# Kernel tuning notes

Measured on AMD Instinct MI355X. Metric: run time of the kernel, lower is better.

Reference implementation:

```python
import jax, jax.numpy as jnp
import numpy as np

B = 256
NUM_IN_CAPS = 1152   # 6*6*32
NUM_OUT_CAPS = 10
VEC_IN = 8
VEC_OUT = 16
ROUTING_ITERS = 3


def squash(x, axis):
    # squash(v) = |v|^2/(1+|v|^2) * v/|v|  (matches torch module, no eps)
    mag_squ = jnp.sum(x * x, axis=axis, keepdims=True)
    return mag_squ / (1.0 + mag_squ) * (x / jnp.sqrt(mag_squ))


def setup_inputs() -> dict:
    key = jax.random.key(0)
    k = jax.random.split(key, 6)
    x = jax.random.normal(k[0], (B, 1, 28, 28), dtype=jnp.float32)
    conv1_w = jax.random.normal(k[1], (256, 1, 9, 9), dtype=jnp.float32) * 0.1
    conv1_b = jnp.zeros((256,), dtype=jnp.float32)
    pc_w = jax.random.normal(k[2], (256, 256, 9, 9), dtype=jnp.float32) * 0.02  # out = 32 caps * 8 dims
    pc_b = jnp.zeros((256,), dtype=jnp.float32)
    # routing transform W: original shape [1,1152,160,8,1] -> [1152,10,16,8]
    W = jax.random.normal(k[3], (NUM_IN_CAPS, NUM_OUT_CAPS, VEC_OUT, VEC_IN), dtype=jnp.float32)
    dc_bias = jnp.zeros((NUM_OUT_CAPS, VEC_OUT), dtype=jnp.float32)
    return {"x": x, "conv1_w": conv1_w, "conv1_b": conv1_b,
            "pc_w": pc_w, "pc_b": pc_b, "W": W, "dc_bias": dc_bias}


def _conv(x, w, b, stride):
    y = jax.lax.conv_general_dilated(x, w, (stride, stride), 'VALID',
                                     dimension_numbers=('NCHW', 'OIHW', 'NCHW'))
    return y + b[None, :, None, None]


def reference(x, conv1_w, conv1_b, pc_w, pc_b, W, dc_bias):
    # conv1: [B,1,28,28] -> [B,256,20,20]  (no activation in original module)
    h = _conv(x, conv1_w, conv1_b, stride=1)
    # primaryCaps conv: -> [B,256,6,6] -> [B,1152,8]
    caps = _conv(h, pc_w, pc_b, stride=2)
    caps = caps.reshape(caps.shape[0], -1, VEC_IN)          # [B,1152,8]
    caps = squash(caps, axis=-1)
    # u_hat[b,i,j,d] = sum_k W[i,j,d,k] * caps[b,i,k]  (the original broadcast-mul-sum)
    u_hat = jnp.einsum('ijdk,bik->bijd', W, caps)           # [B,1152,10,16]
    b_ij = jnp.zeros(u_hat.shape[:3], dtype=u_hat.dtype)    # [B,1152,10]
    for r in range(ROUTING_ITERS):
        c_ij = jax.nn.softmax(b_ij, axis=2)                 # softmax over output caps
        s_j = jnp.einsum('bij,bijd->bjd', c_ij, u_hat) + dc_bias  # [B,10,16]
        v_j = squash(s_j, axis=-1)
        if r != ROUTING_ITERS - 1:
            b_ij = b_ij + jnp.einsum('bijd,bjd->bij', u_hat, v_j)
    return v_j  # [B,10,16]
```

## Files before the change

kernel.cpp:

```cpp
#include <hip/hip_runtime.h>
#include <hip/hip_bf16.h>


typedef __attribute__((ext_vector_type(8))) short short8;
typedef __attribute__((ext_vector_type(4))) float float4v;

__device__ inline float bfu(ushort v){ return __uint_as_float((unsigned)v << 16); }

__global__ __launch_bounds__(640) void conv1_kernel(const float* __restrict__ x,
    const float* __restrict__ w, const float* __restrict__ bias,
    __hip_bfloat16* __restrict__ ht){
  __shared__ float img[784];
  __shared__ float wsv[32 * 81];
  __shared__ ushort tile[400 * 33];
  int b = blockIdx.x;
  int og = blockIdx.y;
  int t = threadIdx.x;
  const float* xb = x + (size_t)b * 784;
  for (int idx = t; idx < 784; idx += 640) img[idx] = xb[idx];
  for (int idx = t; idx < 2592; idx += 640) wsv[idx] = w[(size_t)og * 2592 + idx];
  __syncthreads();
  int o_l = t / 20;
  int y   = t - o_l * 20;
  float acc[20];
  #pragma unroll
  for (int i = 0; i < 20; i++) acc[i] = 0.f;
  #pragma unroll
  for (int r = 0; r < 9; r++){
    float row[28];
    const float4* rp = (const float4*)&img[(y + r) * 28];
    #pragma unroll
    for (int q = 0; q < 7; q++){
      float4 v4 = rp[q];
      row[4*q+0]=v4.x; row[4*q+1]=v4.y; row[4*q+2]=v4.z; row[4*q+3]=v4.w;
    }
    #pragma unroll
    for (int s = 0; s < 9; s++){
      float wv = wsv[o_l * 81 + r * 9 + s];
      #pragma unroll
      for (int xx = 0; xx < 20; xx++)
        acc[xx] = fmaf(wv, row[xx + s], acc[xx]);
    }
  }
  float bv = bias[og * 32 + o_l];
  #pragma unroll
  for (int xx = 0; xx < 20; xx++){
    __hip_bfloat16 hv = __float2bfloat16(acc[xx] + bv);
    tile[(y * 20 + xx) * 33 + o_l] = *(ushort*)&hv;
  }
  __syncthreads();
  __hip_bfloat16* hb = ht + (size_t)b * 102400 + og * 32;
  for (int idx = t; idx < 6400; idx += 640){
    int pos = idx >> 4, op = idx & 15;
    unsigned v = (unsigned)tile[pos * 33 + op * 2]
               | ((unsigned)tile[pos * 33 + op * 2 + 1] << 16);
    *(unsigned*)(hb + (size_t)pos * 256 + op * 2) = v;
  }
}

__global__ __launch_bounds__(256) void arepack_kernel(const float* __restrict__ w2,
    ushort* __restrict__ A2s){
  __shared__ float wbuf[64 * 81];
  int o = blockIdx.x;
  int t = threadIdx.x;
  int ow = o >> 6, fo = (o >> 4) & 3, l15 = o & 15;
  size_t obase8 = (size_t)ow * 165888 + (size_t)fo * 64 + (size_t)l15 * 4;
  for (int c0 = 0; c0 < 256; c0 += 64){
    __syncthreads();
    for (int idx = t; idx < 5184; idx += 256)
      wbuf[idx] = w2[(size_t)o * 20736 + (size_t)c0 * 81 + idx];
    __syncthreads();
    for (int idx = t; idx < 2592; idx += 256){
      int rs = idx >> 5;
      int cp = (idx & 31) * 2;
      int cg = c0 + cp;
      int ct = cg >> 5, quad = (cg >> 3) & 3, e = cg & 7;
      __hip_bfloat16 b0 = __float2bfloat16(wbuf[cp * 81 + rs]);
      __hip_bfloat16 b1 = __float2bfloat16(wbuf[(cp + 1) * 81 + rs]);
      unsigned pack = (unsigned)*(ushort*)&b0 | ((unsigned)*(ushort*)&b1 << 16);
      size_t si = (obase8 + (size_t)ct * 256 + (size_t)rs * 2048 + quad) * 8 + e;
      *(unsigned*)(A2s + si) = pack;
    }
  }
}

__global__ __launch_bounds__(256) void wrepack_kernel(const float* __restrict__ W,
    ushort* __restrict__ Wrb){
  __shared__ float tile[64][65];
  int r0 = blockIdx.x * 64;
  int c0 = blockIdx.y * 64;
  int t = threadIdx.x; int lx = t & 63, ly = t >> 6;
  for (int rr = ly; rr < 64; rr += 4)
    tile[rr][lx] = W[(size_t)(r0 + rr) * 1280 + c0 + lx];
  __syncthreads();
  for (int rr = ly; rr < 64; rr += 4){
    __hip_bfloat16 hv = __float2bfloat16(tile[lx][rr]);
    Wrb[(size_t)(c0 + rr) * 1152 + r0 + lx] = *(ushort*)&hv;
  }
}

__global__ __launch_bounds__(256, 2) void conv2_mfma_kernel(
    const __hip_bfloat16* __restrict__ ht, const short8* __restrict__ A2,
    float* __restrict__ caps4){
  __shared__ ushort img[2][400 * 40];
  int bx  = blockIdx.x;
  int xcd = bx & 7;
  int kq  = xcd >> 1;
  int p   = ((bx >> 3) << 1) | (xcd & 1);
  int b0  = p * 2;
  int t = threadIdx.x;
  int lane = t & 63;
  int wid  = t >> 6;
  int l15  = lane & 15;
  int quad = lane >> 4;

  int bn[3], slc[3];
  #pragma unroll
  for (int fn = 0; fn < 3; fn++){
    int n = fn * 16 + l15;
    int y = n / 6, xx = n - y * 6;
    if (n >= 36){ y = 0; xx = 0; }
    bn[fn]  = 40 * y + 2 * xx;
    slc[fn] = (quad + 4 * y) % 5;
  }
  const short8* i0p = (const short8*)&img[0][0];
  const short8* i1p = (const short8*)&img[1][0];

  float4v acc[4][6];
  #pragma unroll
  for (int fo = 0; fo < 4; fo++)
    #pragma unroll
    for (int fn = 0; fn < 6; fn++)
      acc[fo][fn] = (float4v){0.f, 0.f, 0.f, 0.f};

  for (int ci = 0; ci < 2; ci++){
    int ct = kq * 2 + ci;
    __syncthreads();
    #pragma unroll
    for (int im = 0; im < 2; im++){
      const __hip_bfloat16* hb = ht + (size_t)(b0 + im) * 102400;
      for (int idx = t; idx < 1600; idx += 256){
        int pp = idx >> 2, q = idx & 3;
        int sl = (q + 2 * (pp / 20)) % 5;
        uint4 v = *(const uint4*)(hb + (size_t)pp * 256 + ct * 32 + q * 8);
        *(uint4*)&img[im][pp * 40 + sl * 8] = v;
      }
    }
    __syncthreads();

    const short8* ap = A2 + ((size_t)wid * 648 + ct) * 256 + l15 * 4 + quad;

    short8 aF[2][4], bF[2][6];
    #pragma unroll
    for (int fo = 0; fo < 4; fo++) aF[0][fo] = ap[fo * 64];
    #pragma unroll
    for (int fn = 0; fn < 6; fn++){
      int f3 = (fn < 3) ? fn : fn - 3;
      const short8* ib = (fn < 3) ? i0p : i1p;
      bF[0][fn] = ib[bn[f3] * 5 + slc[f3]];
    }

    int rn = 0, sn = 0, r2m = 0;
    #pragma unroll 2
    for (int rs = 0; rs < 81; rs++){
      int cur = rs & 1, nxt = cur ^ 1;
      sn++;
      if (sn == 9){ sn = 0; rn++; r2m += 2; if (r2m >= 5) r2m -= 5; }
      int nrs = (rs < 80) ? rs + 1 : 80;
      int roff = rn * 20 + sn;
      const short8* apn = ap + (size_t)nrs * 2048;
      #pragma unroll
      for (int fo = 0; fo < 4; fo++) aF[nxt][fo] = apn[fo * 64];
      #pragma unroll
      for (int fn = 0; fn < 6; fn++){
        int f3 = (fn < 3) ? fn : fn - 3;
        const short8* ib = (fn < 3) ? i0p : i1p;
        int sl = slc[f3] + r2m; if (sl >= 5) sl -= 5;
        bF[nxt][fn] = ib[(bn[f3] + roff) * 5 + sl];
      }
      #pragma unroll
      for (int fo = 0; fo < 4; fo++)
        #pragma unroll
        for (int fn = 0; fn < 6; fn++)
          acc[fo][fn] = __builtin_amdgcn_mfma_f32_16x16x32_bf16(aF[cur][fo], bF[cur][fn], acc[fo][fn], 0, 0, 0);
    }
  }

  #pragma unroll
  for (int fn = 0; fn < 6; fn++){
    int im = (fn < 3) ? 0 : 1;
    int f3 = (fn < 3) ? fn : fn - 3;
    int pos = f3 * 16 + l15;
    if (pos < 36){
      float* cb = caps4 + ((size_t)kq * 256 + b0 + im) * 9216;
      #pragma unroll
      for (int fo = 0; fo < 4; fo++){
        int ob = wid * 64 + fo * 16 + quad * 4;
        #pragma unroll
        for (int rr = 0; rr < 4; rr++)
          cb[(size_t)(ob + rr) * 36 + pos] = acc[fo][fn][rr];
      }
    }
  }
}

__global__ __launch_bounds__(256) void squash4_kernel(const float* __restrict__ caps4,
    const float* __restrict__ bias, float* __restrict__ caps){
  size_t cid = (size_t)blockIdx.x * 256 + threadIdx.x;
  size_t base = cid * 8;
  const size_t STR = 2359296;
  float4 a0 = *(const float4*)(caps4 + base);
  float4 a1 = *(const float4*)(caps4 + base + 4);
  #pragma unroll
  for (int k = 1; k < 4; k++){
    float4 q0 = *(const float4*)(caps4 + k * STR + base);
    float4 q1 = *(const float4*)(caps4 + k * STR + base + 4);
    a0.x+=q0.x; a0.y+=q0.y; a0.z+=q0.z; a0.w+=q0.w;
    a1.x+=q1.x; a1.y+=q1.y; a1.z+=q1.z; a1.w+=q1.w;
  }
  int off = (int)(base % 9216);
  float v[8] = {a0.x,a0.y,a0.z,a0.w,a1.x,a1.y,a1.z,a1.w};
  #pragma unroll
  for (int e = 0; e < 8; e++) v[e] += bias[(off + e) / 36];
  float msq = 0.f;
  #pragma unroll
  for (int e = 0; e < 8; e++) msq += v[e]*v[e];
  float scale = sqrtf(msq) / (1.f + msq);
  float* cp = caps + base;
  #pragma unroll
  for (int e = 0; e < 8; e++) cp[e] = v[e]*scale;
}

__global__ __launch_bounds__(256) void uhat_t_kernel(const float* __restrict__ caps,
    const ushort* __restrict__ Wrb, ushort* __restrict__ uT){
  __shared__ float cl[8 * 16 * 64];
  int i0  = blockIdx.x * 64;
  int by  = blockIdx.y;
  int b0  = (by >> 2) * 16;
  int jd0 = (by & 3) * 40;
  int t = threadIdx.x, lane = t & 63, w = t >> 6;
  for (int f = t; f < 2048; f += 256){
    int base = f * 4; int bb = base >> 9; int r = base & 511;
    int il = r >> 3; int k = r & 7;
    float4 v = *(const float4*)(caps + ((size_t)(b0+bb)*1152 + i0 + il)*8 + k);
    cl[((k+0)*16+bb)*64+il] = v.x;
    cl[((k+1)*16+bb)*64+il] = v.y;
    cl[((k+2)*16+bb)*64+il] = v.z;
    cl[((k+3)*16+bb)*64+il] = v.w;
  }
  __syncthreads();
  for (int jj = 0; jj < 10; jj++){
    int jd = jd0 + w * 10 + jj;
    float wk[8];
    #pragma unroll
    for (int k = 0; k < 8; k++)
      wk[k] = bfu(Wrb[((size_t)jd * 8 + k) * 1152 + i0 + lane]);
    #pragma unroll
    for (int bb = 0; bb < 16; bb++){
      float acc = 0.f;
      #pragma unroll
      for (int k = 0; k < 8; k++) acc = fmaf(wk[k], cl[(k*16+bb)*64+lane], acc);
      __hip_bfloat16 hv = __float2bfloat16(acc);
      uT[((size_t)(b0+bb)*160 + jd)*1152 + i0 + lane] = *(ushort*)&hv;
    }
  }
}

__global__ __launch_bounds__(384) void routeAB_kernel(
    const ushort* __restrict__ uT, const float* __restrict__ vin,
    float* __restrict__ bbuf, float* __restrict__ spart, int mode){
  __shared__ float c_l[384 * 11];
  __shared__ float vs[160];
  int ic = blockIdx.x;
  int b  = blockIdx.y;
  int t = threadIdx.x;
  int lane = t & 63, w = t >> 6;
  const ushort* ub = uT + (size_t)b * 184320 + ic * 384;

  if (mode){
    if (t < 160) vs[t] = vin[b * 160 + t];
    __syncthreads();
    const ushort* up = ub + t;
    float d[10];
    #pragma unroll
    for (int j = 0; j < 10; j++){
      float dj = 0.f;
      #pragma unroll
      for (int dd = 0; dd < 16; dd++){
        int jd = j * 16 + dd;
        dj = fmaf(bfu(up[(size_t)jd * 1152]), vs[jd], dj);
      }
      d[j] = dj;
    }
    float* bp = bbuf + ((size_t)b * 1152 + ic * 384 + t) * 10;
    if (mode == 2){
      #pragma unroll
      for (int j = 0; j < 10; j++) d[j] += bp[j];
    } else {
      #pragma unroll
      for (int j = 0; j < 10; j++) bp[j] = d[j];
    }
    float m = d[0];
    #pragma unroll
    for (int j = 1; j < 10; j++) m = fmaxf(m, d[j]);
    float se = 0.f;
    #pragma unroll
    for (int j = 0; j < 10; j++){ d[j] = __expf(d[j] - m); se += d[j]; }
    float inv = 1.f / se;
    #pragma unroll
    for (int j = 0; j < 10; j++) c_l[t * 11 + j] = d[j] * inv;
  }
  __syncthreads();

  for (int jd = w; jd < 160; jd += 6){
    const uint* urow32 = (const uint*)(ub + (size_t)jd * 1152);
    float sacc = 0.f;
    if (mode){
      int jj = jd >> 4;
      #pragma unroll
      for (int st = 0; st < 3; st++){
        uint uv = urow32[st * 64 + lane];
        int i_l = (st * 64 + lane) * 2;
        sacc = fmaf(bfu((ushort)(uv & 0xffffu)), c_l[i_l * 11 + jj], sacc);
        sacc = fmaf(bfu((ushort)(uv >> 16)),     c_l[(i_l + 1) * 11 + jj], sacc);
      }
    } else {
      #pragma unroll
      for (int st = 0; st < 3; st++){
        uint uv = urow32[st * 64 + lane];
        sacc += bfu((ushort)(uv & 0xffffu)) + bfu((ushort)(uv >> 16));
      }
    }
    sacc += __shfl_xor(sacc, 32);
    sacc += __shfl_xor(sacc, 16);
    sacc += __shfl_xor(sacc, 8);
    sacc += __shfl_xor(sacc, 4);
    sacc += __shfl_xor(sacc, 2);
    sacc += __shfl_xor(sacc, 1);
    if (lane == 0) spart[((size_t)ic * 256 + b) * 160 + jd] = mode ? sacc : sacc * 0.1f;
  }
}

__global__ __launch_bounds__(160) void vsq_kernel(const float* __restrict__ spart,
    const float* __restrict__ dcb, float* __restrict__ vout){
  int b = blockIdx.x;
  int t = threadIdx.x;
  float s = dcb[t];
  #pragma unroll
  for (int ic = 0; ic < 3; ic++) s += spart[((size_t)ic * 256 + b) * 160 + t];
  float msq = s * s;
  msq += __shfl_xor(msq, 1, 16);
  msq += __shfl_xor(msq, 2, 16);
  msq += __shfl_xor(msq, 4, 16);
  msq += __shfl_xor(msq, 8, 16);
  float scale = sqrtf(msq) / (1.f + msq);
  vout[b * 160 + t] = s * scale;
}

extern "C" void kernel_launch(void* const* d_in, const int* in_sizes, int n_in,
                              void* d_out, int out_size, void* d_ws, size_t ws_size,
                              hipStream_t stream){
  (void)in_sizes; (void)n_in; (void)out_size; (void)ws_size;
  const float* x   = (const float*)d_in[0];
  const float* w1  = (const float*)d_in[1];
  const float* b1  = (const float*)d_in[2];
  const float* w2  = (const float*)d_in[3];
  const float* b2  = (const float*)d_in[4];
  const float* W   = (const float*)d_in[5];
  const float* dcb = (const float*)d_in[6];
  float* out = (float*)d_out;

  char* ws = (char*)d_ws;
  __hip_bfloat16* ht = (__hip_bfloat16*)(ws);
  ushort* A2s  = (ushort*)(ws + 52428800);
  float* caps4 = (float*)(ws + 63045632);
  ushort* uT   = (ushort*)(ws);
  float* caps  = (float*)(ws + 100794368);
  ushort* Wrb  = (ushort*)(ws + 110231552);
  float* bbuf  = (float*)(ws + 113180672);
  float* spart = (float*)(ws + 124977152);
  float* vbuf  = (float*)(ws + 125468672);

  conv1_kernel<<<dim3(256, 8), 640, 0, stream>>>(x, w1, b1, ht);
  arepack_kernel<<<256, 256, 0, stream>>>(w2, A2s);
  wrepack_kernel<<<dim3(18, 20), 256, 0, stream>>>(W, Wrb);
  conv2_mfma_kernel<<<512, 256, 0, stream>>>(ht, (const short8*)A2s, caps4);
  squash4_kernel<<<1152, 256, 0, stream>>>(caps4, b2, caps);
  uhat_t_kernel<<<dim3(18, 64), 256, 0, stream>>>(caps, Wrb, uT);
  routeAB_kernel<<<dim3(3, 256), 384, 0, stream>>>(uT, vbuf, bbuf, spart, 0);
  vsq_kernel<<<256, 160, 0, stream>>>(spart, dcb, vbuf);
  routeAB_kernel<<<dim3(3, 256), 384, 0, stream>>>(uT, vbuf, bbuf, spart, 1);
  vsq_kernel<<<256, 160, 0, stream>>>(spart, dcb, vbuf);
  routeAB_kernel<<<dim3(3, 256), 384, 0, stream>>>(uT, vbuf, bbuf, spart, 2);
  vsq_kernel<<<256, 160, 0, stream>>>(spart, dcb, out);
}
```

Measured before the change: 392.7 us.

## Stage u_hat tile in LDS and split routing into nine chunks

The routing kernel now stages each block's 160x128 bf16 u_hat slice into shared memory with coalesced 32-bit loads. Both the agreement dot product and the weighted sum then read it from LDS instead of reading global memory twice. The grid grows from 3 to 9 input-capsule chunks per batch with 256 threads, so vsq sums 9 partials and vbuf moves to make room. This aims to cut duplicated global traffic and strided loads and to raise parallelism, at the cost of about 43KB of LDS per block and more partial-sum traffic.

```diff
diff --git a/kernel.cpp b/kernel.cpp
--- a/kernel.cpp
+++ b/kernel.cpp
@@ -266,70 +266,75 @@
   }
 }
 
-__global__ __launch_bounds__(384) void routeAB_kernel(
+__global__ __launch_bounds__(256) void routeAB_kernel(
     const ushort* __restrict__ uT, const float* __restrict__ vin,
     float* __restrict__ bbuf, float* __restrict__ spart, int mode){
-  __shared__ float c_l[384 * 11];
+  __shared__ ushort u_c[160 * 136];
+  __shared__ float c_l[128 * 11];
   __shared__ float vs[160];
   int ic = blockIdx.x;
   int b  = blockIdx.y;
   int t = threadIdx.x;
   int lane = t & 63, w = t >> 6;
-  const ushort* ub = uT + (size_t)b * 184320 + ic * 384;
+  int i0 = ic * 128;
+
+  const uint* ug = (const uint*)(uT + (size_t)b * 184320) + (i0 >> 1);
+  uint* u32 = (uint*)u_c;
+  #pragma unroll 8
+  for (int step = 0; step < 40; step++){
+    int jd = step * 4 + w;
+    u32[jd * 68 + lane] = ug[(size_t)jd * 576 + lane];
+  }
+  if (mode && t < 160) vs[t] = vin[b * 160 + t];
+  __syncthreads();
 
   if (mode){
-    if (t < 160) vs[t] = vin[b * 160 + t];
+    if (t < 128){
+      float d[10];
+      #pragma unroll
+      for (int j = 0; j < 10; j++){
+        float dj = 0.f;
+        #pragma unroll
+        for (int dd = 0; dd < 16; dd++){
+          int jd = j * 16 + dd;
+          dj = fmaf(bfu(u_c[jd * 136 + t]), vs[jd], dj);
+        }
+        d[j] = dj;
+      }
+      float* bp = bbuf + ((size_t)b * 1152 + i0 + t) * 10;
+      if (mode == 2){
+        #pragma unroll
+        for (int j = 0; j < 10; j++) d[j] += bp[j];
+      } else {
+        #pragma unroll
+        for (int j = 0; j < 10; j++) bp[j] = d[j];
+      }
+      float m = d[0];
+      #pragma unroll
+      for (int j = 1; j < 10; j++) m = fmaxf(m, d[j]);
+      float se = 0.f;
+      #pragma unroll
+      for (int j = 0; j < 10; j++){ d[j] = __expf(d[j] - m); se += d[j]; }
+      float inv = 1.f / se;
+      #pragma unroll
+      for (int j = 0; j < 10; j++) c_l[t * 11 + j] = d[j] * inv;
+    }
     __syncthreads();
-    const ushort* up = ub + t;
-    float d[10];
-    #pragma unroll
-    for (int j = 0; j < 10; j++){
-      float dj = 0.f;
-      #pragma unroll
-      for (int dd = 0; dd < 16; dd++){
-        int jd = j * 16 + dd;
-        dj = fmaf(bfu(up[(size_t)jd * 1152]), vs[jd], dj);
-      }
-      d[j] = dj;
-    }
-    float* bp = bbuf + ((size_t)b * 1152 + ic * 384 + t) * 10;
-    if (mode == 2){
-      #pragma unroll
-      for (int j = 0; j < 10; j++) d[j] += bp[j];
-    } else {
-      #pragma unroll
-      for (int j = 0; j < 10; j++) bp[j] = d[j];
-    }
-    float m = d[0];
-    #pragma unroll
-    for (int j = 1; j < 10; j++) m = fmaxf(m, d[j]);
-    float se = 0.f;
-    #pragma unroll
-    for (int j = 0; j < 10; j++){ d[j] = __expf(d[j] - m); se += d[j]; }
-    float inv = 1.f / se;
-    #pragma unroll
-    for (int j = 0; j < 10; j++) c_l[t * 11 + j] = d[j] * inv;
-  }
-  __syncthreads();
-
-  for (int jd = w; jd < 160; jd += 6){
-    const uint* urow32 = (const uint*)(ub + (size_t)jd * 1152);
+  }
+
+  for (int jd = w; jd < 160; jd += 4){
     float sacc = 0.f;
     if (mode){
       int jj = jd >> 4;
       #pragma unroll
-      for (int st = 0; st < 3; st++){
-        uint uv = urow32[st * 64 + lane];
-        int i_l = (st * 64 + lane) * 2;
-        sacc = fmaf(bfu((ushort)(uv & 0xffffu)), c_l[i_l * 11 + jj], sacc);
-        sacc = fmaf(bfu((ushort)(uv >> 16)),     c_l[(i_l + 1) * 11 + jj], sacc);
+      for (int st = 0; st < 2; st++){
+        int i_l = st * 64 + lane;
+        sacc = fmaf(bfu(u_c[jd * 136 + i_l]), c_l[i_l * 11 + jj], sacc);
       }
     } else {
       #pragma unroll
-      for (int st = 0; st < 3; st++){
-        uint uv = urow32[st * 64 + lane];
-        sacc += bfu((ushort)(uv & 0xffffu)) + bfu((ushort)(uv >> 16));
-      }
+      for (int st = 0; st < 2; st++)
+        sacc += bfu(u_c[jd * 136 + st * 64 + lane]);
     }
     sacc += __shfl_xor(sacc, 32);
     sacc += __shfl_xor(sacc, 16);
@@ -347,7 +352,7 @@
   int t = threadIdx.x;
   float s = dcb[t];
   #pragma unroll
-  for (int ic = 0; ic < 3; ic++) s += spart[((size_t)ic * 256 + b) * 160 + t];
+  for (int ic = 0; ic < 9; ic++) s += spart[((size_t)ic * 256 + b) * 160 + t];
   float msq = s * s;
   msq += __shfl_xor(msq, 1, 16);
   msq += __shfl_xor(msq, 2, 16);
@@ -379,7 +384,7 @@
   ushort* Wrb  = (ushort*)(ws + 110231552);
   float* bbuf  = (float*)(ws + 113180672);
   float* spart = (float*)(ws + 124977152);
-  float* vbuf  = (float*)(ws + 125468672);
+  float* vbuf  = (float*)(ws + 126451712);
 
   conv1_kernel<<<dim3(256, 8), 640, 0, stream>>>(x, w1, b1, ht);
   arepack_kernel<<<256, 256, 0, stream>>>(w2, A2s);
@@ -387,10 +392,10 @@
   conv2_mfma_kernel<<<512, 256, 0, stream>>>(ht, (const short8*)A2s, caps4);
   squash4_kernel<<<1152, 256, 0, stream>>>(caps4, b2, caps);
   uhat_t_kernel<<<dim3(18, 64), 256, 0, stream>>>(caps, Wrb, uT);
-  routeAB_kernel<<<dim3(3, 256), 384, 0, stream>>>(uT, vbuf, bbuf, spart, 0);
+  routeAB_kernel<<<dim3(9, 256), 256, 0, stream>>>(uT, vbuf, bbuf, spart, 0);
   vsq_kernel<<<256, 160, 0, stream>>>(spart, dcb, vbuf);
-  routeAB_kernel<<<dim3(3, 256), 384, 0, stream>>>(uT, vbuf, bbuf, spart, 1);
+  routeAB_kernel<<<dim3(9, 256), 256, 0, stream>>>(uT, vbuf, bbuf, spart, 1);
   vsq_kernel<<<256, 160, 0, stream>>>(spart, dcb, vbuf);
-  routeAB_kernel<<<dim3(3, 256), 384, 0, stream>>>(uT, vbuf, bbuf, spart, 2);
+  routeAB_kernel<<<dim3(9, 256), 256, 0, stream>>>(uT, vbuf, bbuf, spart, 2);
   vsq_kernel<<<256, 160, 0, stream>>>(spart, dcb, out);
 }
```

Result: slower. 483.2 us (+23.0%).

## Fuse first routing iteration's uniform-weight sum into u_hat kernel

Applied to the files above, without the earlier changes.

The first routing pass uses uniform coupling (0.1), so its s_j partial sums are now computed inside uhat_t_kernel by wave-reducing the fp32 products before the bf16 store. A new vsq0 kernel combines the 18 partials per batch item. This drops one full routeAB pass over uT, which removes a read of roughly 94 MB of bf16 data. In exchange it adds shuffle reductions and an extra sync in uhat, and the first-pass sums now come from fp32 values instead of bf16-rounded ones.

```diff
diff --git a/kernel.cpp b/kernel.cpp
--- a/kernel.cpp
+++ b/kernel.cpp
@@ -232,8 +232,10 @@
 }
 
 __global__ __launch_bounds__(256) void uhat_t_kernel(const float* __restrict__ caps,
-    const ushort* __restrict__ Wrb, ushort* __restrict__ uT){
+    const ushort* __restrict__ Wrb, ushort* __restrict__ uT,
+    float* __restrict__ spart0){
   __shared__ float cl[8 * 16 * 64];
+  __shared__ float sred[16][40];
   int i0  = blockIdx.x * 64;
   int by  = blockIdx.y;
   int b0  = (by >> 2) * 16;
@@ -250,7 +252,8 @@
   }
   __syncthreads();
   for (int jj = 0; jj < 10; jj++){
-    int jd = jd0 + w * 10 + jj;
+    int jdl = w * 10 + jj;
+    int jd  = jd0 + jdl;
     float wk[8];
     #pragma unroll
     for (int k = 0; k < 8; k++)
@@ -262,8 +265,38 @@
       for (int k = 0; k < 8; k++) acc = fmaf(wk[k], cl[(k*16+bb)*64+lane], acc);
       __hip_bfloat16 hv = __float2bfloat16(acc);
       uT[((size_t)(b0+bb)*160 + jd)*1152 + i0 + lane] = *(ushort*)&hv;
-    }
-  }
+      float r = acc;
+      r += __shfl_xor(r, 32);
+      r += __shfl_xor(r, 16);
+      r += __shfl_xor(r, 8);
+      r += __shfl_xor(r, 4);
+      r += __shfl_xor(r, 2);
+      r += __shfl_xor(r, 1);
+      if (lane == 0) sred[bb][jdl] = r;
+    }
+  }
+  __syncthreads();
+  for (int f = t; f < 640; f += 256){
+    int bb = f / 40, jj = f - bb * 40;
+    spart0[((size_t)blockIdx.x * 256 + b0 + bb) * 160 + jd0 + jj] = sred[bb][jj];
+  }
+}
+
+__global__ __launch_bounds__(160) void vsq0_kernel(const float* __restrict__ spart0,
+    const float* __restrict__ dcb, float* __restrict__ vout){
+  int b = blockIdx.x;
+  int t = threadIdx.x;
+  float s = 0.f;
+  #pragma unroll
+  for (int ic = 0; ic < 18; ic++) s += spart0[((size_t)ic * 256 + b) * 160 + t];
+  s = 0.1f * s + dcb[t];
+  float msq = s * s;
+  msq += __shfl_xor(msq, 1, 16);
+  msq += __shfl_xor(msq, 2, 16);
+  msq += __shfl_xor(msq, 4, 16);
+  msq += __shfl_xor(msq, 8, 16);
+  float scale = sqrtf(msq) / (1.f + msq);
+  vout[b * 160 + t] = s * scale;
 }
 
 __global__ __launch_bounds__(384) void routeAB_kernel(
@@ -277,9 +310,9 @@
   int lane = t & 63, w = t >> 6;
   const ushort* ub = uT + (size_t)b * 184320 + ic * 384;
 
-  if (mode){
-    if (t < 160) vs[t] = vin[b * 160 + t];
-    __syncthreads();
+  if (t < 160) vs[t] = vin[b * 160 + t];
+  __syncthreads();
+  {
     const ushort* up = ub + t;
     float d[10];
     #pragma unroll
@@ -315,21 +348,13 @@
   for (int jd = w; jd < 160; jd += 6){
     const uint* urow32 = (const uint*)(ub + (size_t)jd * 1152);
     float sacc = 0.f;
-    if (mode){
-      int jj = jd >> 4;
-      #pragma unroll
-      for (int st = 0; st < 3; st++){
-        uint uv = urow32[st * 64 + lane];
-        int i_l = (st * 64 + lane) * 2;
-        sacc = fmaf(bfu((ushort)(uv & 0xffffu)), c_l[i_l * 11 + jj], sacc);
-        sacc = fmaf(bfu((ushort)(uv >> 16)),     c_l[(i_l + 1) * 11 + jj], sacc);
-      }
-    } else {
-      #pragma unroll
-      for (int st = 0; st < 3; st++){
-        uint uv = urow32[st * 64 + lane];
-        sacc += bfu((ushort)(uv & 0xffffu)) + bfu((ushort)(uv >> 16));
-      }
+    int jj = jd >> 4;
+    #pragma unroll
+    for (int st = 0; st < 3; st++){
+      uint uv = urow32[st * 64 + lane];
+      int i_l = (st * 64 + lane) * 2;
+      sacc = fmaf(bfu((ushort)(uv & 0xffffu)), c_l[i_l * 11 + jj], sacc);
+      sacc = fmaf(bfu((ushort)(uv >> 16)),     c_l[(i_l + 1) * 11 + jj], sacc);
     }
     sacc += __shfl_xor(sacc, 32);
     sacc += __shfl_xor(sacc, 16);
@@ -337,7 +362,7 @@
     sacc += __shfl_xor(sacc, 4);
     sacc += __shfl_xor(sacc, 2);
     sacc += __shfl_xor(sacc, 1);
-    if (lane == 0) spart[((size_t)ic * 256 + b) * 160 + jd] = mode ? sacc : sacc * 0.1f;
+    if (lane == 0) spart[((size_t)ic * 256 + b) * 160 + jd] = sacc;
   }
 }
 
@@ -372,23 +397,23 @@
 
   char* ws = (char*)d_ws;
   __hip_bfloat16* ht = (__hip_bfloat16*)(ws);
-  ushort* A2s  = (ushort*)(ws + 52428800);
-  float* caps4 = (float*)(ws + 63045632);
-  ushort* uT   = (ushort*)(ws);
-  float* caps  = (float*)(ws + 100794368);
-  ushort* Wrb  = (ushort*)(ws + 110231552);
-  float* bbuf  = (float*)(ws + 113180672);
-  float* spart = (float*)(ws + 124977152);
-  float* vbuf  = (float*)(ws + 125468672);
+  ushort* A2s   = (ushort*)(ws + 52428800);
+  float* caps4  = (float*)(ws + 63045632);
+  ushort* uT    = (ushort*)(ws);
+  float* caps   = (float*)(ws + 100794368);
+  ushort* Wrb   = (ushort*)(ws + 110231552);
+  float* bbuf   = (float*)(ws + 113180672);
+  float* spart  = (float*)(ws + 124977152);
+  float* spart0 = (float*)(ws + 125468672);
+  float* vbuf   = (float*)(ws + 128417792);
 
   conv1_kernel<<<dim3(256, 8), 640, 0, stream>>>(x, w1, b1, ht);
   arepack_kernel<<<256, 256, 0, stream>>>(w2, A2s);
   wrepack_kernel<<<dim3(18, 20), 256, 0, stream>>>(W, Wrb);
   conv2_mfma_kernel<<<512, 256, 0, stream>>>(ht, (const short8*)A2s, caps4);
   squash4_kernel<<<1152, 256, 0, stream>>>(caps4, b2, caps);
-  uhat_t_kernel<<<dim3(18, 64), 256, 0, stream>>>(caps, Wrb, uT);
-  routeAB_kernel<<<dim3(3, 256), 384, 0, stream>>>(uT, vbuf, bbuf, spart, 0);
-  vsq_kernel<<<256, 160, 0, stream>>>(spart, dcb, vbuf);
+  uhat_t_kernel<<<dim3(18, 64), 256, 0, stream>>>(caps, Wrb, uT, spart0);
+  vsq0_kernel<<<256, 160, 0, stream>>>(spart0, dcb, vbuf);
   routeAB_kernel<<<dim3(3, 256), 384, 0, stream>>>(uT, vbuf, bbuf, spart, 1);
   vsq_kernel<<<256, 160, 0, stream>>>(spart, dcb, vbuf);
   routeAB_kernel<<<dim3(3, 256), 384, 0, stream>>>(uT, vbuf, bbuf, spart, 2);
```

Measured after the change: 438.3 us. +11.6%, slower.
